# Performance work log

Hardware: AMD Instinct MI355X
Metric: run time of the kernel (lower is better)

## Reference

```python
import jax, jax.numpy as jnp
import numpy as np

DIM = 2048
HID = 1024
E = 16
TOP_K = 2
S_SHARED = 2


def setup_inputs() -> dict:
    key = jax.random.key(0)
    ks = jax.random.split(key, 6)
    scale = 0.02
    x = jax.random.normal(ks[0], (2, 2048, DIM), dtype=jnp.float32)
    gate_w = jax.random.normal(ks[1], (DIM, E), dtype=jnp.float32) * scale
    shared_w1 = jax.random.normal(ks[2], (S_SHARED, DIM, HID), dtype=jnp.float32) * scale
    shared_w2 = jax.random.normal(ks[3], (S_SHARED, HID, DIM), dtype=jnp.float32) * scale
    w1 = jax.random.normal(ks[4], (E, DIM, HID), dtype=jnp.float32) * scale
    w2 = jax.random.normal(ks[5], (E, HID, DIM), dtype=jnp.float32) * scale
    return {"x": x, "gate_w": gate_w, "shared_w1": shared_w1,
            "shared_w2": shared_w2, "w1": w1, "w2": w2}


def reference(x, gate_w, shared_w1, shared_w2, w1, w2):
    orig_shape = x.shape
    xf = x.reshape(-1, orig_shape[-1])  # [T, D]

    # Shared experts: sum of SiLU MLPs
    hs = jax.nn.silu(jnp.einsum('td,sdh->sth', xf, shared_w1))
    shared_out = jnp.einsum('sth,shd->td', hs, shared_w2)

    # Gating
    probs = jax.nn.softmax(xf @ gate_w, axis=-1)              # [T, E]
    weights, indices = jax.lax.top_k(probs, TOP_K)            # [T, K]
    weights = weights / weights.sum(axis=-1, keepdims=True)
    aux_loss = (probs.mean(axis=0) ** 2).sum() * E

    # Combine weights per (token, expert): top_k indices are distinct
    combine = (jax.nn.one_hot(indices, E, dtype=xf.dtype) *
               weights[..., None]).sum(axis=1)                # [T, E]

    # Dense all-expert compute (reference form of gather-GEMM-scatter)
    h = jax.nn.silu(jnp.einsum('td,edh->eth', xf, w1))        # [E, T, H]
    y = jnp.einsum('eth,ehd->etd', h, w2)                     # [E, T, D]
    routed_out = jnp.einsum('te,etd->td', combine, y)         # [T, D]

    out = (shared_out + routed_out).reshape(orig_shape)
    return out, aux_loss
```

## Files before the change

kernel.cpp:

```cpp
#include <hip/hip_runtime.h>
#include <math.h>

typedef unsigned short u16;
typedef __bf16 bf16x8 __attribute__((ext_vector_type(8)));
typedef float f32x4 __attribute__((ext_vector_type(4)));

#define T_TOK 4096
#define DIMD 2048
#define HIDD 1024
#define NEXP 16
#define RMAX 10240
#define MAXBLK 96
#define BM 128
#define BN 256
#define BK 64

__device__ __forceinline__ u16 f2b(float f) {
  unsigned u = __builtin_bit_cast(unsigned, f);
  unsigned r = (u + 0x7FFFu + ((u >> 16) & 1u)) >> 16;
  return (u16)r;
}

__device__ __forceinline__ void gld16(const void* g, void* l) {
  __builtin_amdgcn_global_load_lds(
      (const __attribute__((address_space(1))) void*)g,
      (__attribute__((address_space(3))) void*)l, 16, 0, 0);
}


__global__ void k_zero(float* __restrict__ o) {
  const int i = blockIdx.x * blockDim.x + threadIdx.x;
  float4 z = {0.f, 0.f, 0.f, 0.f};
  ((float4*)o)[i] = z;
}

__global__ void k_init(int* perm, int* cnt, int* fill) {
  int i = blockIdx.x * blockDim.x + threadIdx.x;
  if (i < RMAX) perm[i] = -1;
  if (i < NEXP) { cnt[i] = 0; fill[i] = 0; }
}

__global__ void k_cvt(const float* __restrict__ x, u16* __restrict__ xb) {
  const int i = blockIdx.x * blockDim.x + threadIdx.x;
  const float4 v = ((const float4*)x)[i];
  union { u16 u[4]; unsigned long long q; } t;
  t.u[0] = f2b(v.x); t.u[1] = f2b(v.y); t.u[2] = f2b(v.z); t.u[3] = f2b(v.w);
  ((unsigned long long*)xb)[i] = t.q;
}

__global__ __launch_bounds__(256)
void k_tr(const float* __restrict__ W, u16* __restrict__ Wt,
          int K, int N, long estride, int ld_out) {
  __shared__ float t[64][65];
  const int e = blockIdx.z;
  const float* Win = W + (size_t)e * (size_t)K * (size_t)N;
  u16* Wo = Wt + (size_t)e * (size_t)estride;
  const int n0 = blockIdx.x * 64, k0 = blockIdx.y * 64;
  const int r = threadIdx.x >> 4;
  const int c = (threadIdx.x & 15) * 4;
#pragma unroll
  for (int p = 0; p < 4; ++p) {
    const int kk = p * 16 + r;
    const float4 v = *(const float4*)&Win[(size_t)(k0 + kk) * N + n0 + c];
    t[kk][c] = v.x; t[kk][c + 1] = v.y; t[kk][c + 2] = v.z; t[kk][c + 3] = v.w;
  }
  __syncthreads();
#pragma unroll
  for (int p = 0; p < 4; ++p) {
    const int nn = p * 16 + r;
    ushort4 o;
    o.x = f2b(t[c + 0][nn]); o.y = f2b(t[c + 1][nn]);
    o.z = f2b(t[c + 2][nn]); o.w = f2b(t[c + 3][nn]);
    *(ushort4*)&Wo[(size_t)(n0 + nn) * ld_out + k0 + c] = o;
  }
}

__global__ __launch_bounds__(256)
void k_gate(const float* __restrict__ x, const float* __restrict__ gw,
            int* __restrict__ top2i, float* __restrict__ top2w,
            int* __restrict__ cnt, float* __restrict__ partial) {
  const int e = threadIdx.x & 15;
  const int tt = threadIdx.x >> 4;
  const int t = blockIdx.x * 16 + tt;
  const float* xp = x + (size_t)t * DIMD;
  float acc = 0.f;
#pragma unroll 8
  for (int k = 0; k < DIMD; ++k) acc = fmaf(xp[k], gw[k * NEXP + e], acc);
  __shared__ float lg[16][17];
  __shared__ float pr[16][17];
  lg[tt][e] = acc;
  __syncthreads();
  if (e == 0) {
    float l[16];
    float mx = -1e30f;
    for (int j = 0; j < 16; ++j) { l[j] = lg[tt][j]; mx = fmaxf(mx, l[j]); }
    float s = 0.f;
    for (int j = 0; j < 16; ++j) { l[j] = expf(l[j] - mx); s += l[j]; }
    const float inv = 1.f / s;
    float p1 = -1.f, p2 = -1.f; int i1 = 0, i2 = 0;
    for (int j = 0; j < 16; ++j) {
      const float p = l[j] * inv;
      pr[tt][j] = p;
      if (p > p1) { p2 = p1; i2 = i1; p1 = p; i1 = j; }
      else if (p > p2) { p2 = p; i2 = j; }
    }
    const float wsum = p1 + p2;
    top2i[t * 2 + 0] = i1;
    top2i[t * 2 + 1] = i2;
    top2w[t * 2 + 0] = p1 / wsum;
    top2w[t * 2 + 1] = p2 / wsum;
    atomicAdd(&cnt[i1], 1);
    atomicAdd(&cnt[i2], 1);
  }
  __syncthreads();
  if (tt == 0) {
    float s = 0.f;
    for (int j = 0; j < 16; ++j) s += pr[j][e];
    partial[blockIdx.x * 16 + e] = s;
  }
}

__global__ __launch_bounds__(256)
void k_aux(const float* __restrict__ partial, float* __restrict__ auxOut) {
  __shared__ float s[16][17];
  const int e = threadIdx.x & 15, c = threadIdx.x >> 4;
  float a = 0.f;
  for (int b = c; b < 256; b += 16) a += partial[b * 16 + e];
  s[c][e] = a;
  __syncthreads();
  if (threadIdx.x == 0) {
    float aux = 0.f;
    for (int j = 0; j < 16; ++j) {
      float tot = 0.f;
      for (int cc = 0; cc < 16; ++cc) tot += s[cc][j];
      const float m = tot / (float)T_TOK;
      aux += m * m;
    }
    auxOut[0] = aux * (float)NEXP;
  }
}

__global__ void k_off(const int* __restrict__ cnt, int* __restrict__ offs,
                      int* __restrict__ tbl_e, int* __restrict__ tbl_r0,
                      int* __restrict__ nblk) {
  if (threadIdx.x != 0 || blockIdx.x != 0) return;
  int o = 0, nb = 0;
  for (int e = 0; e < NEXP; ++e) {
    offs[e] = o;
    const int b = (cnt[e] + BM - 1) / BM;
    for (int i = 0; i < b; ++i) { tbl_e[nb] = e; tbl_r0[nb] = o + i * BM; ++nb; }
    o += b * BM;
  }
  offs[NEXP] = o;
  nblk[0] = nb;
}

__global__ void k_fill(const int* __restrict__ top2i, const float* __restrict__ top2w,
                       const int* __restrict__ offs, int* __restrict__ fill,
                       int* __restrict__ perm, float* __restrict__ wrow) {
  const int id = blockIdx.x * blockDim.x + threadIdx.x;
  if (id >= T_TOK * 2) return;
  const int e = top2i[id];
  const int pos = atomicAdd(&fill[e], 1);
  const int r = offs[e] + pos;
  perm[r] = id >> 1;
  wrow[r] = top2w[id];
}


__device__ __forceinline__ void stage_tile(
    const u16* gA0, const u16* gA1, const u16* gB0, const u16* gB1,
    const u16* gB2, const u16* gB3, int k0, u16* S, int b, int w) {
  u16* As = S + b * 24576;
  u16* Bs = As + 8192;
  gld16(gA0 + k0, As + w * 512);
  gld16(gA1 + k0, As + 4096 + w * 512);
  gld16(gB0 + k0, Bs + w * 512);
  gld16(gB1 + k0, Bs + 4096 + w * 512);
  gld16(gB2 + k0, Bs + 8192 + w * 512);
  gld16(gB3 + k0, Bs + 12288 + w * 512);
}

__device__ __forceinline__ void comp_tile(const u16* __restrict__ S, int b,
    const int (&aoff)[4][2], const int (&boff)[4][2], f32x4 (&acc)[4][4]) {
  const u16* As = S + b * 24576;
  const u16* Bs = As + 8192;
#pragma unroll
  for (int kh = 0; kh < 2; ++kh) {
    bf16x8 a[4], bq[4];
#pragma unroll
    for (int i = 0; i < 4; ++i) a[i] = *(const bf16x8*)(As + aoff[i][kh]);
#pragma unroll
    for (int j = 0; j < 4; ++j) bq[j] = *(const bf16x8*)(Bs + boff[j][kh]);
    __builtin_amdgcn_s_setprio(1);
#pragma unroll
    for (int i = 0; i < 4; ++i)
#pragma unroll
      for (int j = 0; j < 4; ++j)
        acc[i][j] = __builtin_amdgcn_mfma_f32_16x16x32_bf16(a[i], bq[j], acc[i][j], 0, 0, 0);
    __builtin_amdgcn_s_setprio(0);
  }
}

#define FENCE asm volatile("" ::: "memory")
#define VMW6  asm volatile("s_waitcnt vmcnt(6)" ::: "memory")
#define VMW0  asm volatile("s_waitcnt vmcnt(0)" ::: "memory")

__device__ __forceinline__ void gemm_pipe(
    const u16* gA0, const u16* gA1, const u16* gB0, const u16* gB1,
    const u16* gB2, const u16* gB3, int K, u16* S,
    const int (&aoff)[4][2], const int (&boff)[4][2],
    f32x4 (&acc)[4][4], int w) {
  const int nt = K >> 6;
  stage_tile(gA0, gA1, gB0, gB1, gB2, gB3, 0, S, 0, w);
  stage_tile(gA0, gA1, gB0, gB1, gB2, gB3, 64, S, 1, w);
  VMW6;
  __builtin_amdgcn_s_barrier();
  FENCE;
  for (int t = 0; t < nt - 2; ++t) {
    comp_tile(S, t & 1, aoff, boff, acc);
    FENCE;
    __builtin_amdgcn_s_barrier();
    FENCE;
    stage_tile(gA0, gA1, gB0, gB1, gB2, gB3, (t + 2) << 6, S, t & 1, w);
    VMW6;
    __builtin_amdgcn_s_barrier();
    FENCE;
  }
  comp_tile(S, 0, aoff, boff, acc);
  VMW0;
  __builtin_amdgcn_s_barrier();
  FENCE;
  comp_tile(S, 1, aoff, boff, acc);
}

__global__ __launch_bounds__(512, 2)
void k_up(const u16* __restrict__ xb, const u16* __restrict__ sw1t,
          const u16* __restrict__ w1t, u16* __restrict__ hbS,
          u16* __restrict__ hbR, const int* __restrict__ perm,
          const int* __restrict__ tbl_e, const int* __restrict__ tbl_r0,
          const int* __restrict__ nblk) {
  __shared__ u16 S[49152];
  const int bx = blockIdx.x, by = blockIdx.y;
  const int tid = threadIdx.x;
  const int w = tid >> 6, lane = tid & 63;
  const int lm = lane & 15, lq = lane >> 4;
  const int wm = w >> 2, wn = w & 3;
  const int srow = w * 8 + (lane >> 3);
  const int c8 = lane & 7;

  const bool routed = bx >= 32;
  int r0, ga0, ga1;
  const u16* Bb;
  if (!routed) {
    r0 = bx * BM;
    Bb = sw1t;
    ga0 = r0 + srow; ga1 = r0 + 64 + srow;
  } else {
    if (by >= 4) return;
    const int rbx = bx - 32;
    if (rbx >= *nblk) return;
    const int e = tbl_e[rbx];
    r0 = tbl_r0[rbx];
    Bb = w1t + (size_t)e * (size_t)HIDD * DIMD;
    const int p0 = perm[r0 + srow];      ga0 = (p0 < 0) ? 0 : p0;
    const int p1 = perm[r0 + 64 + srow]; ga1 = (p1 < 0) ? 0 : p1;
  }
  const int n0 = by * BN;
  const u16* gA0 = xb + (size_t)ga0 * DIMD + (c8 ^ ((srow >> 1) & 7)) * 8;
  const u16* gA1 = xb + (size_t)ga1 * DIMD + (c8 ^ (((64 + srow) >> 1) & 7)) * 8;
  const u16* gB[4];
#pragma unroll
  for (int p = 0; p < 4; ++p) {
    const int n = p * 64 + srow;
    gB[p] = Bb + (size_t)(n0 + n) * DIMD + (c8 ^ ((n >> 1) & 7)) * 8;
  }
  int aoff[4][2], boff[4][2];
#pragma unroll
  for (int i = 0; i < 4; ++i) {
    const int m = wm * 64 + i * 16 + lm;
    const int n = wn * 64 + i * 16 + lm;
#pragma unroll
    for (int kh = 0; kh < 2; ++kh) {
      aoff[i][kh] = m * 64 + (((kh << 2) | lq) ^ ((m >> 1) & 7)) * 8;
      boff[i][kh] = n * 64 + (((kh << 2) | lq) ^ ((n >> 1) & 7)) * 8;
    }
  }
  f32x4 acc[4][4];
#pragma unroll
  for (int i = 0; i < 4; ++i)
#pragma unroll
    for (int j = 0; j < 4; ++j) {
      acc[i][j][0] = 0.f; acc[i][j][1] = 0.f; acc[i][j][2] = 0.f; acc[i][j][3] = 0.f;
    }

  gemm_pipe(gA0, gA1, gB[0], gB[1], gB[2], gB[3], DIMD, S, aoff, boff, acc, w);

#pragma unroll
  for (int i = 0; i < 4; ++i) {
#pragma unroll
    for (int r = 0; r < 4; ++r) {
      const int row = r0 + wm * 64 + i * 16 + lq * 4 + r;
      u16* dst = routed ? &hbR[(size_t)row * HIDD] : &hbS[(size_t)row * DIMD];
#pragma unroll
      for (int j = 0; j < 4; ++j) {
        const int gc = n0 + wn * 64 + j * 16 + lm;
        const float v = acc[i][j][r];
        const float s = v / (1.f + expf(-v));
        dst[gc] = f2b(s);
      }
    }
  }
}

__global__ __launch_bounds__(512, 2)
void k_down(const u16* __restrict__ hbS, const u16* __restrict__ hbR,
            const u16* __restrict__ sw2ct, const u16* __restrict__ w2t,
            float* __restrict__ out, const int* __restrict__ perm,
            const float* __restrict__ wrow,
            const int* __restrict__ tbl_e, const int* __restrict__ tbl_r0,
            const int* __restrict__ nblk) {
  __shared__ u16 S[49152];
  const int bx = blockIdx.x, by = blockIdx.y;
  const int tid = threadIdx.x;
  const int w = tid >> 6, lane = tid & 63;
  const int lm = lane & 15, lq = lane >> 4;
  const int wm = w >> 2, wn = w & 3;
  const int srow = w * 8 + (lane >> 3);
  const int c8 = lane & 7;

  const bool routed = bx >= 32;
  int r0, K, ld;
  const u16 *Ab, *Bb;
  if (!routed) {
    r0 = bx * BM;
    Ab = hbS; K = DIMD; ld = DIMD;
    Bb = sw2ct;
  } else {
    const int rbx = bx - 32;
    if (rbx >= *nblk) return;
    const int e = tbl_e[rbx];
    r0 = tbl_r0[rbx];
    Ab = hbR; K = HIDD; ld = HIDD;
    Bb = w2t + (size_t)e * (size_t)DIMD * HIDD;
  }
  const int n0 = by * BN;
  const u16* gA0 = Ab + (size_t)(r0 + srow) * ld + (c8 ^ ((srow >> 1) & 7)) * 8;
  const u16* gA1 = Ab + (size_t)(r0 + 64 + srow) * ld + (c8 ^ (((64 + srow) >> 1) & 7)) * 8;
  const u16* gB[4];
#pragma unroll
  for (int p = 0; p < 4; ++p) {
    const int n = p * 64 + srow;
    gB[p] = Bb + (size_t)(n0 + n) * ld + (c8 ^ ((n >> 1) & 7)) * 8;
  }
  int aoff[4][2], boff[4][2];
#pragma unroll
  for (int i = 0; i < 4; ++i) {
    const int m = wm * 64 + i * 16 + lm;
    const int n = wn * 64 + i * 16 + lm;
#pragma unroll
    for (int kh = 0; kh < 2; ++kh) {
      aoff[i][kh] = m * 64 + (((kh << 2) | lq) ^ ((m >> 1) & 7)) * 8;
      boff[i][kh] = n * 64 + (((kh << 2) | lq) ^ ((n >> 1) & 7)) * 8;
    }
  }
  f32x4 acc[4][4];
#pragma unroll
  for (int i = 0; i < 4; ++i)
#pragma unroll
    for (int j = 0; j < 4; ++j) {
      acc[i][j][0] = 0.f; acc[i][j][1] = 0.f; acc[i][j][2] = 0.f; acc[i][j][3] = 0.f;
    }

  gemm_pipe(gA0, gA1, gB[0], gB[1], gB[2], gB[3], K, S, aoff, boff, acc, w);

#pragma unroll
  for (int i = 0; i < 4; ++i) {
#pragma unroll
    for (int r = 0; r < 4; ++r) {
      const int rr = r0 + wm * 64 + i * 16 + lq * 4 + r;
      int t; float wt;
      if (!routed) { t = rr; wt = 1.f; }
      else { t = perm[rr]; wt = (t >= 0) ? wrow[rr] : 0.f; }
      if (t >= 0) {
        float* dst = &out[(size_t)t * DIMD];
#pragma unroll
        for (int j = 0; j < 4; ++j) {
          const int gc = n0 + wn * 64 + j * 16 + lm;
          atomicAdd(&dst[gc], wt * acc[i][j][r]);
        }
      }
    }
  }
}


extern "C" void kernel_launch(void* const* d_in, const int* in_sizes, int n_in,
                              void* d_out, int out_size, void* d_ws, size_t ws_size,
                              hipStream_t stream) {
  const float* x   = (const float*)d_in[0];
  const float* gw  = (const float*)d_in[1];
  const float* sw1 = (const float*)d_in[2];
  const float* sw2 = (const float*)d_in[3];
  const float* w1  = (const float*)d_in[4];
  const float* w2  = (const float*)d_in[5];
  float* out = (float*)d_out;

  char* ws = (char*)d_ws;
  u16* xb    = (u16*)(ws);
  u16* hbS   = (u16*)(ws + (size_t)( 16 << 20));
  u16* hbR   = (u16*)(ws + (size_t)( 32 << 20));
  u16* sw1t  = (u16*)(ws + (size_t)( 56 << 20));
  u16* sw2ct = (u16*)(ws + (size_t)( 64 << 20));
  u16* w1t   = (u16*)(ws + (size_t)( 72 << 20));
  u16* w2t   = (u16*)(ws + (size_t)(136 << 20));
  char* p = ws + (size_t)(200 << 20);
  int*   top2i   = (int*)p;    p += T_TOK * 2 * 4;
  float* top2w   = (float*)p;  p += T_TOK * 2 * 4;
  int*   perm    = (int*)p;    p += RMAX * 4;
  float* wrow    = (float*)p;  p += RMAX * 4;
  int*   cnt     = (int*)p;    p += 16 * 4;
  int*   fill    = (int*)p;    p += 16 * 4;
  int*   offs    = (int*)p;    p += 32 * 4;
  int*   tbl_e   = (int*)p;    p += MAXBLK * 4;
  int*   tbl_r0  = (int*)p;    p += MAXBLK * 4;
  int*   nblk    = (int*)p;    p += 16 * 4;
  float* partial = (float*)p;  p += 256 * 16 * 4;

  k_zero<<<(T_TOK * DIMD / 4) / 256, 256, 0, stream>>>(out);
  k_init<<<(RMAX + 255) / 256, 256, 0, stream>>>(perm, cnt, fill);
  k_cvt<<<(T_TOK * DIMD / 4) / 256, 256, 0, stream>>>(x, xb);
  k_gate<<<T_TOK / 16, 256, 0, stream>>>(x, gw, top2i, top2w, cnt, partial);
  k_off<<<1, 64, 0, stream>>>(cnt, offs, tbl_e, tbl_r0, nblk);
  k_fill<<<(T_TOK * 2 + 255) / 256, 256, 0, stream>>>(top2i, top2w, offs, fill, perm, wrow);
  k_aux<<<1, 256, 0, stream>>>(partial, out + (size_t)T_TOK * DIMD);

  k_tr<<<dim3(1024 / 64, 2048 / 64,  2), 256, 0, stream>>>(sw1, sw1t, 2048, 1024, 1024l * 2048, 2048);
  k_tr<<<dim3(2048 / 64, 1024 / 64,  2), 256, 0, stream>>>(sw2, sw2ct, 1024, 2048, 1024, 2048);
  k_tr<<<dim3(1024 / 64, 2048 / 64, 16), 256, 0, stream>>>(w1, w1t, 2048, 1024, 1024l * 2048, 2048);
  k_tr<<<dim3(2048 / 64, 1024 / 64, 16), 256, 0, stream>>>(w2, w2t, 1024, 2048, 2048l * 1024, 1024);

  k_up<<<dim3(32 + MAXBLK, 8), 512, 0, stream>>>(xb, sw1t, w1t, hbS, hbR,
                                                 perm, tbl_e, tbl_r0, nblk);
  k_down<<<dim3(32 + MAXBLK, 8), 512, 0, stream>>>(hbS, hbR, sw2ct, w2t, out,
                                                   perm, wrow, tbl_e, tbl_r0, nblk);
}
```

Baseline: 813.4 us.

## Triple-buffer GEMM LDS pipeline and swap grid axes for N-fastest block order

The GEMM mainloop moves from double to triple buffering: three K-tiles are staged ahead, with a wait of vmcnt(12) so two tiles stay in flight, and LDS per block grows to 144 KB. The launch grid is transposed so N-tiles vary fastest within a row block. Consecutive blocks then share the same A rows (gathered tokens), which should improve cache reuse. Routed up-projection blocks are spread across the 8 x-slots by parity, covering their 4 N-tiles. The larger LDS footprint may limit blocks per CU to one, even though launch bounds still request two, so occupancy is at risk.

```diff
diff --git a/kernel.cpp b/kernel.cpp
--- a/kernel.cpp
+++ b/kernel.cpp
@@ -203,6 +203,7 @@
 }
 
 #define FENCE asm volatile("" ::: "memory")
+#define VMW12 asm volatile("s_waitcnt vmcnt(12)" ::: "memory")
 #define VMW6  asm volatile("s_waitcnt vmcnt(6)" ::: "memory")
 #define VMW0  asm volatile("s_waitcnt vmcnt(0)" ::: "memory")
 
@@ -214,24 +215,35 @@
   const int nt = K >> 6;
   stage_tile(gA0, gA1, gB0, gB1, gB2, gB3, 0, S, 0, w);
   stage_tile(gA0, gA1, gB0, gB1, gB2, gB3, 64, S, 1, w);
+  stage_tile(gA0, gA1, gB0, gB1, gB2, gB3, 128, S, 2, w);
+  VMW12;
+  __builtin_amdgcn_s_barrier();
+  FENCE;
+  int b = 0;
+  for (int t = 0; t < nt - 3; ++t) {
+    comp_tile(S, b, aoff, boff, acc);
+    FENCE;
+    __builtin_amdgcn_s_barrier();
+    FENCE;
+    stage_tile(gA0, gA1, gB0, gB1, gB2, gB3, (t + 3) << 6, S, b, w);
+    VMW12;
+    __builtin_amdgcn_s_barrier();
+    FENCE;
+    b = (b == 2) ? 0 : b + 1;
+  }
+  comp_tile(S, b, aoff, boff, acc);
+  FENCE;
   VMW6;
   __builtin_amdgcn_s_barrier();
   FENCE;
-  for (int t = 0; t < nt - 2; ++t) {
-    comp_tile(S, t & 1, aoff, boff, acc);
-    FENCE;
-    __builtin_amdgcn_s_barrier();
-    FENCE;
-    stage_tile(gA0, gA1, gB0, gB1, gB2, gB3, (t + 2) << 6, S, t & 1, w);
-    VMW6;
-    __builtin_amdgcn_s_barrier();
-    FENCE;
-  }
-  comp_tile(S, 0, aoff, boff, acc);
+  b = (b == 2) ? 0 : b + 1;
+  comp_tile(S, b, aoff, boff, acc);
+  FENCE;
   VMW0;
   __builtin_amdgcn_s_barrier();
   FENCE;
-  comp_tile(S, 1, aoff, boff, acc);
+  b = (b == 2) ? 0 : b + 1;
+  comp_tile(S, b, aoff, boff, acc);
 }
 
 __global__ __launch_bounds__(512, 2)
@@ -240,7 +252,7 @@
           u16* __restrict__ hbR, const int* __restrict__ perm,
           const int* __restrict__ tbl_e, const int* __restrict__ tbl_r0,
           const int* __restrict__ nblk) {
-  __shared__ u16 S[49152];
+  __shared__ u16 S[73728];
   const int bx = blockIdx.x, by = blockIdx.y;
   const int tid = threadIdx.x;
   const int w = tid >> 6, lane = tid & 63;
@@ -249,24 +261,25 @@
   const int srow = w * 8 + (lane >> 3);
   const int c8 = lane & 7;
 
-  const bool routed = bx >= 32;
-  int r0, ga0, ga1;
+  const bool routed = by >= 32;
+  int r0, n0, ga0, ga1;
   const u16* Bb;
   if (!routed) {
-    r0 = bx * BM;
+    r0 = by * BM;
+    n0 = bx * BN;
     Bb = sw1t;
     ga0 = r0 + srow; ga1 = r0 + 64 + srow;
   } else {
-    if (by >= 4) return;
-    const int rbx = bx - 32;
+    const int rbx = by - 32;
     if (rbx >= *nblk) return;
+    if ((rbx & 1) != (bx & 1)) return;
+    n0 = (bx >> 1) * BN;
     const int e = tbl_e[rbx];
     r0 = tbl_r0[rbx];
     Bb = w1t + (size_t)e * (size_t)HIDD * DIMD;
     const int p0 = perm[r0 + srow];      ga0 = (p0 < 0) ? 0 : p0;
     const int p1 = perm[r0 + 64 + srow]; ga1 = (p1 < 0) ? 0 : p1;
   }
-  const int n0 = by * BN;
   const u16* gA0 = xb + (size_t)ga0 * DIMD + (c8 ^ ((srow >> 1) & 7)) * 8;
   const u16* gA1 = xb + (size_t)ga1 * DIMD + (c8 ^ (((64 + srow) >> 1) & 7)) * 8;
   const u16* gB[4];
@@ -320,7 +333,7 @@
             const float* __restrict__ wrow,
             const int* __restrict__ tbl_e, const int* __restrict__ tbl_r0,
             const int* __restrict__ nblk) {
-  __shared__ u16 S[49152];
+  __shared__ u16 S[73728];
   const int bx = blockIdx.x, by = blockIdx.y;
   const int tid = threadIdx.x;
   const int w = tid >> 6, lane = tid & 63;
@@ -329,22 +342,22 @@
   const int srow = w * 8 + (lane >> 3);
   const int c8 = lane & 7;
 
-  const bool routed = bx >= 32;
+  const bool routed = by >= 32;
   int r0, K, ld;
   const u16 *Ab, *Bb;
   if (!routed) {
-    r0 = bx * BM;
+    r0 = by * BM;
     Ab = hbS; K = DIMD; ld = DIMD;
     Bb = sw2ct;
   } else {
-    const int rbx = bx - 32;
+    const int rbx = by - 32;
     if (rbx >= *nblk) return;
     const int e = tbl_e[rbx];
     r0 = tbl_r0[rbx];
     Ab = hbR; K = HIDD; ld = HIDD;
     Bb = w2t + (size_t)e * (size_t)DIMD * HIDD;
   }
-  const int n0 = by * BN;
+  const int n0 = bx * BN;
   const u16* gA0 = Ab + (size_t)(r0 + srow) * ld + (c8 ^ ((srow >> 1) & 7)) * 8;
   const u16* gA1 = Ab + (size_t)(r0 + 64 + srow) * ld + (c8 ^ (((64 + srow) >> 1) & 7)) * 8;
   const u16* gB[4];
@@ -440,8 +453,8 @@
   k_tr<<<dim3(1024 / 64, 2048 / 64, 16), 256, 0, stream>>>(w1, w1t, 2048, 1024, 1024l * 2048, 2048);
   k_tr<<<dim3(2048 / 64, 1024 / 64, 16), 256, 0, stream>>>(w2, w2t, 1024, 2048, 2048l * 1024, 1024);
 
-  k_up<<<dim3(32 + MAXBLK, 8), 512, 0, stream>>>(xb, sw1t, w1t, hbS, hbR,
+  k_up<<<dim3(8, 32 + MAXBLK), 512, 0, stream>>>(xb, sw1t, w1t, hbS, hbR,
                                                  perm, tbl_e, tbl_r0, nblk);
-  k_down<<<dim3(32 + MAXBLK, 8), 512, 0, stream>>>(hbS, hbR, sw2ct, w2t, out,
+  k_down<<<dim3(8, 32 + MAXBLK), 512, 0, stream>>>(hbS, hbR, sw2ct, w2t, out,
                                                    perm, wrow, tbl_e, tbl_r0, nblk);
 }
```

Result: slower. 852.2 us (+4.8%).
